# Performance work log

Hardware: AMD Instinct MI355X
Metric: run time of the kernel (lower is better)

The kernel has to match this reference:

```python
import jax, jax.numpy as jnp
import numpy as np

THRESHOLD = 0.7


def ternary_dequant(w, threshold=THRESHOLD):
    """Ternary quantize {-1,0,+1} with masked-mean alpha, return ternary*alpha."""
    abs_w = jnp.abs(w)
    delta = threshold * jnp.mean(abs_w)
    ternary = jnp.where(w > delta, 1.0, jnp.where(w < -delta, -1.0, 0.0)).astype(w.dtype)
    nz = ternary != 0
    cnt = jnp.sum(nz)
    # alpha = mean(|w| over nonzero ternary entries); fall back to mean(|w|) if all-zero
    masked_sum = jnp.sum(jnp.where(nz, abs_w, 0.0))
    alpha = jnp.where(cnt > 0, masked_sum / jnp.maximum(cnt, 1).astype(w.dtype), jnp.mean(abs_w))
    return ternary * alpha


def setup_inputs() -> dict:
    key = jax.random.key(0)
    kx, kw, kb = jax.random.split(key, 3)
    B, S, D_IN, D_OUT = 4, 2048, 4096, 4096
    x = jax.random.normal(kx, (B * S, D_IN), dtype=jnp.float32)
    # xavier-uniform-ish init for latent FP32 weights
    limit = np.sqrt(6.0 / (D_IN + D_OUT)).astype(np.float32)
    weight = jax.random.uniform(kw, (D_OUT, D_IN), dtype=jnp.float32, minval=-limit, maxval=limit)
    bias = jax.random.normal(kb, (D_OUT,), dtype=jnp.float32) * 0.02
    return {"x": x, "weight": weight, "bias": bias}


def reference(x, weight, bias):
    q_weight = ternary_dequant(weight)  # (out, in)
    return jnp.matmul(x, q_weight.T) + bias  # (tokens, out)
```

## Files before the change

### kernel.cpp

```cpp
#include <hip/hip_runtime.h>

#define M_DIM 8192
#define N_DIM 4096
#define K_DIM 4096

typedef __attribute__((ext_vector_type(8))) __bf16 bf16x8;
typedef __attribute__((ext_vector_type(4))) __bf16 bf16x4;
typedef __attribute__((ext_vector_type(4))) float floatx4;

__device__ __forceinline__ void async_copy16(const void* g, void* l) {
    __builtin_amdgcn_global_load_lds(
        (const __attribute__((address_space(1))) void*)g,
        (__attribute__((address_space(3))) void*)l,
        16, 0, 0);
}

__device__ __forceinline__ unsigned lds_addr(const void* p) {
    return (unsigned)(unsigned long long)(const __attribute__((address_space(3))) void*)p;
}
__device__ __forceinline__ bf16x8 lds_read_b128(unsigned addr) {
    bf16x8 r;
    asm volatile("ds_read_b128 %0, %1" : "=v"(r) : "v"(addr));
    return r;
}

__device__ __forceinline__ double wave_reduce_d(double v) {
    #pragma unroll
    for (int o = 32; o > 0; o >>= 1) v += __shfl_down(v, o, 64);
    return v;
}
__device__ __forceinline__ unsigned wave_reduce_u(unsigned v) {
    #pragma unroll
    for (int o = 32; o > 0; o >>= 1) v += __shfl_down(v, o, 64);
    return v;
}

__global__ __launch_bounds__(256) void k_pre(const float4* __restrict__ w4,
                                             double* __restrict__ part,
                                             const float4* __restrict__ x4,
                                             bf16x4* __restrict__ xb) {
    const int tid = threadIdx.x;
    if (blockIdx.x < 2048) {
        int idx = blockIdx.x * 256 + tid;
        double s = 0.0;
        #pragma unroll
        for (int it = 0; it < 8; ++it) {
            float4 v = w4[idx + it * (2048 * 256)];
            s += (double)fabsf(v.x) + (double)fabsf(v.y) +
                 (double)fabsf(v.z) + (double)fabsf(v.w);
        }
        s = wave_reduce_d(s);
        __shared__ double sm[4];
        if ((tid & 63) == 0) sm[tid >> 6] = s;
        __syncthreads();
        if (tid == 0) part[blockIdx.x] = sm[0] + sm[1] + sm[2] + sm[3];
    } else {
        int idx = (blockIdx.x - 2048) * 256 + tid;
        #pragma unroll
        for (int it = 0; it < 4; ++it) {
            int i = idx + it * (8192 * 256);
            float4 v = x4[i];
            bf16x4 o;
            o[0] = (__bf16)v.x; o[1] = (__bf16)v.y;
            o[2] = (__bf16)v.z; o[3] = (__bf16)v.w;
            xb[i] = o;
        }
    }
}

__global__ __launch_bounds__(256) void k_quant(const float4* __restrict__ w4,
                                               bf16x4* __restrict__ tern,
                                               const double* __restrict__ part,
                                               double* __restrict__ scal,
                                               double* __restrict__ pm,
                                               unsigned* __restrict__ pc) {
    const int tid = threadIdx.x;
    double s = 0.0;
    #pragma unroll
    for (int i = 0; i < 8; ++i) s += part[tid + i * 256];
    s = wave_reduce_d(s);
    __shared__ double sm[4];
    if ((tid & 63) == 0) sm[tid >> 6] = s;
    __syncthreads();
    const double mean = (sm[0] + sm[1] + sm[2] + sm[3]) * (1.0 / 16777216.0);
    const double delta = 0.7 * mean;
    if (blockIdx.x == 0 && tid == 0) scal[0] = mean;

    int idx = blockIdx.x * 256 + tid;
    double msum = 0.0;
    unsigned cnt = 0;
    #pragma unroll
    for (int it = 0; it < 8; ++it) {
        int i = idx + it * (2048 * 256);
        float4 v = w4[i];
        float e[4] = {v.x, v.y, v.z, v.w};
        bf16x4 o;
        #pragma unroll
        for (int c = 0; c < 4; ++c) {
            float wv = e[c];
            float t = ((double)wv > delta) ? 1.0f
                    : (((double)wv < -delta) ? -1.0f : 0.0f);
            if (t != 0.0f) { msum += (double)fabsf(wv); cnt++; }
            o[c] = (__bf16)t;
        }
        tern[i] = o;
    }
    msum = wave_reduce_d(msum);
    cnt  = wave_reduce_u(cnt);
    __shared__ double smd[4];
    __shared__ unsigned smu[4];
    if ((tid & 63) == 0) { smd[tid >> 6] = msum; smu[tid >> 6] = cnt; }
    __syncthreads();
    if (tid == 0) {
        pm[blockIdx.x] = smd[0] + smd[1] + smd[2] + smd[3];
        pc[blockIdx.x] = smu[0] + smu[1] + smu[2] + smu[3];
    }
}

__global__ __launch_bounds__(512, 2) void ternary_gemm(
    const __bf16* __restrict__ A,
    const __bf16* __restrict__ B,
    const float*  __restrict__ bias,
    const double* __restrict__ scal,
    const double* __restrict__ pm,
    const unsigned* __restrict__ pc,
    float* __restrict__ C)
{
    __shared__ __attribute__((aligned(128))) __bf16 As[4][8192];
    __shared__ __attribute__((aligned(128))) __bf16 Bs[4][8192];
    __shared__ double smd[8];
    __shared__ unsigned smu[8];

    const int tid  = threadIdx.x;
    const int w    = tid >> 6;
    const int lane = tid & 63;
    const int quad = lane >> 4;
    const int l16  = lane & 15;
    const int wr = w >> 2;
    const int wc = w & 3;

    const int id = (blockIdx.x & 7) * 64 + (blockIdx.x >> 3);
    const int br = id >> 4;
    const int bc = id & 15;

    const int srow = lane >> 2;
    const int scol = ((lane & 3) ^ ((srow >> 1) & 3)) * 8;

    const __bf16* gA0 = A + (size_t)(br * 256 + w * 16 + srow) * K_DIM + scol;
    const __bf16* gA1 = gA0 + (size_t)128 * K_DIM;
    const __bf16* gB0 = B + (size_t)(bc * 256 + w * 16 + srow) * K_DIM + scol;
    const __bf16* gB1 = gB0 + (size_t)128 * K_DIM;

    floatx4 acc[8][4] = {};

    const int swz   = (quad ^ ((l16 >> 1) & 3)) * 8;
    const int a_off = (wr * 128 + l16) * 32 + swz;
    const int b_off = (wc * 64 + l16) * 32 + swz;

    const unsigned aAddr0 = lds_addr(&As[0][0]) + (unsigned)(a_off * 2);
    const unsigned bAddr0 = lds_addr(&Bs[0][0]) + (unsigned)(b_off * 2);

#define STAGE_A(ktt) do {                                        \
        const int _sb = (ktt) & 3; const int _so = (ktt) * 32;   \
        async_copy16(gA0 + _so, &As[_sb][w * 512]);              \
        async_copy16(gA1 + _so, &As[_sb][(w + 8) * 512]);        \
    } while (0)
#define STAGE_B(ktt) do {                                        \
        const int _sb = (ktt) & 3; const int _so = (ktt) * 32;   \
        async_copy16(gB0 + _so, &Bs[_sb][w * 512]);              \
        async_copy16(gB1 + _so, &Bs[_sb][(w + 8) * 512]);        \
    } while (0)

    STAGE_A(0); STAGE_B(0);
    STAGE_A(1); STAGE_B(1);
    STAGE_A(2); STAGE_B(2);

#define TILE(kt_, VMN, DO_STAGE_) do {                                         \
        asm volatile("s_waitcnt vmcnt(" #VMN ")" ::: "memory");                \
        __builtin_amdgcn_s_barrier();                                          \
        const unsigned _bufB = (unsigned)(((kt_) & 3) * 16384);                \
        bf16x8 _a[8], _b[4];                                                   \
        _Pragma("unroll")                                                      \
        for (int i = 0; i < 4; ++i)                                            \
            _a[i] = lds_read_b128(aAddr0 + _bufB + (unsigned)(i * 1024));      \
        _Pragma("unroll")                                                      \
        for (int j = 0; j < 4; ++j)                                            \
            _b[j] = lds_read_b128(bAddr0 + _bufB + (unsigned)(j * 1024));      \
        _Pragma("unroll")                                                      \
        for (int i = 4; i < 8; ++i)                                            \
            _a[i] = lds_read_b128(aAddr0 + _bufB + (unsigned)(i * 1024));      \
        if (DO_STAGE_) { STAGE_A((kt_) + 3); STAGE_B((kt_) + 3); }             \
        asm volatile("s_waitcnt lgkmcnt(4)" ::: "memory");                     \
        __builtin_amdgcn_sched_barrier(0);                                     \
        __builtin_amdgcn_s_setprio(1);                                         \
        _Pragma("unroll")                                                      \
        for (int i = 0; i < 4; ++i)                                            \
            _Pragma("unroll")                                                  \
            for (int j = 0; j < 4; ++j)                                        \
                acc[i][j] = __builtin_amdgcn_mfma_f32_16x16x32_bf16(           \
                    _a[i], _b[j], acc[i][j], 0, 0, 0);                         \
        __builtin_amdgcn_s_setprio(0);                                         \
        asm volatile("s_waitcnt lgkmcnt(0)" ::: "memory");                     \
        __builtin_amdgcn_sched_barrier(0);                                     \
        __builtin_amdgcn_s_setprio(1);                                         \
        _Pragma("unroll")                                                      \
        for (int i = 0; i < 4; ++i)                                            \
            _Pragma("unroll")                                                  \
            for (int j = 0; j < 4; ++j)                                        \
                acc[4 + i][j] = __builtin_amdgcn_mfma_f32_16x16x32_bf16(       \
                    _a[4 + i], _b[j], acc[4 + i][j], 0, 0, 0);                 \
        __builtin_amdgcn_s_setprio(0);                                         \
        __builtin_amdgcn_sched_barrier(0);                                     \
    } while (0)

    for (int kt = 0; kt < 125; ++kt) TILE(kt, 8, true);
    TILE(125, 8, false);
    TILE(126, 4, false);
    TILE(127, 0, false);

#undef TILE
#undef STAGE_A
#undef STAGE_B

    double s = 0.0; unsigned c = 0;
    #pragma unroll
    for (int i = 0; i < 4; ++i) { s += pm[tid + i * 512]; c += pc[tid + i * 512]; }
    s = wave_reduce_d(s);
    c = wave_reduce_u(c);
    if (lane == 0) { smd[w] = s; smu[w] = c; }
    __syncthreads();
    double ms = 0.0; unsigned ct = 0;
    #pragma unroll
    for (int i = 0; i < 8; ++i) { ms += smd[i]; ct += smu[i]; }
    const float alpha = (float)(ct > 0 ? ms / (double)ct : scal[0]);

    float bv[4];
    #pragma unroll
    for (int j = 0; j < 4; ++j)
        bv[j] = bias[bc * 256 + wc * 64 + j * 16 + l16];

    #pragma unroll
    for (int i = 0; i < 8; ++i) {
        const int row0 = br * 256 + wr * 128 + i * 16 + quad * 4;
        #pragma unroll
        for (int j = 0; j < 4; ++j) {
            const int col = bc * 256 + wc * 64 + j * 16 + l16;
            #pragma unroll
            for (int r = 0; r < 4; ++r)
                C[(size_t)(row0 + r) * N_DIM + col] = acc[i][j][r] * alpha + bv[j];
        }
    }
}

extern "C" void kernel_launch(void* const* d_in, const int* in_sizes, int n_in,
                              void* d_out, int out_size, void* d_ws, size_t ws_size,
                              hipStream_t stream) {
    const float* x    = (const float*)d_in[0];
    const float* w    = (const float*)d_in[1];
    const float* bias = (const float*)d_in[2];
    float* out = (float*)d_out;

    char* ws = (char*)d_ws;
    double*   d_scal = (double*)ws;
    double*   part   = (double*)(ws + 64);
    double*   pm     = (double*)(ws + 16448);
    unsigned* pc     = (unsigned*)(ws + 32832);
    __bf16*   xb     = (__bf16*)(ws + 65536);
    __bf16*   tern   = (__bf16*)(ws + 65536 + (size_t)M_DIM * K_DIM * 2);

    k_pre<<<10240, 256, 0, stream>>>((const float4*)w, part, (const float4*)x, (bf16x4*)xb);
    k_quant<<<2048, 256, 0, stream>>>((const float4*)w, (bf16x4*)tern, part, d_scal, pm, pc);

    dim3 grid(512);
    ternary_gemm<<<grid, 512, 0, stream>>>(xb, tern, bias, d_scal, pm, pc, out);
}
```

Before: 516.3 us.

## Shrink GEMM tile to 256x128 with 4 waves and 3-stage LDS pipeline

Changes the GEMM block tile from 256x256 with 8 waves to 256x128 with 4 waves over 1024 blocks. The LDS ring drops from 4 to 3 stages, with staging issued at the top of each tile and a second barrier at the end of each tile. LDS reads now use immediate offsets instead of computed addresses. Smaller LDS use per block may let more blocks fit per CU, but each block reuses A less, so more bytes of A are fetched per unit of compute, and the extra barrier adds sync cost.

```diff
diff --git a/kernel.cpp b/kernel.cpp
--- a/kernel.cpp
+++ b/kernel.cpp
@@ -18,11 +18,8 @@
 __device__ __forceinline__ unsigned lds_addr(const void* p) {
     return (unsigned)(unsigned long long)(const __attribute__((address_space(3))) void*)p;
 }
-__device__ __forceinline__ bf16x8 lds_read_b128(unsigned addr) {
-    bf16x8 r;
-    asm volatile("ds_read_b128 %0, %1" : "=v"(r) : "v"(addr));
-    return r;
-}
+#define DSR(dst, addr, OFF) \
+    asm volatile("ds_read_b128 %0, %1 offset:" #OFF : "=v"(dst) : "v"(addr))
 
 __device__ __forceinline__ double wave_reduce_d(double v) {
     #pragma unroll
@@ -117,7 +114,7 @@
     }
 }
 
-__global__ __launch_bounds__(512, 2) void ternary_gemm(
+__global__ __launch_bounds__(256, 2) void ternary_gemm(
     const __bf16* __restrict__ A,
     const __bf16* __restrict__ B,
     const float*  __restrict__ bias,
@@ -126,30 +123,34 @@
     const unsigned* __restrict__ pc,
     float* __restrict__ C)
 {
-    __shared__ __attribute__((aligned(128))) __bf16 As[4][8192];
-    __shared__ __attribute__((aligned(128))) __bf16 Bs[4][8192];
-    __shared__ double smd[8];
-    __shared__ unsigned smu[8];
+    __shared__ __attribute__((aligned(128))) __bf16 As[3][8192];
+    __shared__ __attribute__((aligned(128))) __bf16 Bs[3][4096];
+    __shared__ double smd[4];
+    __shared__ unsigned smu[4];
 
     const int tid  = threadIdx.x;
     const int w    = tid >> 6;
     const int lane = tid & 63;
     const int quad = lane >> 4;
     const int l16  = lane & 15;
-    const int wr = w >> 2;
-    const int wc = w & 3;
-
-    const int id = (blockIdx.x & 7) * 64 + (blockIdx.x >> 3);
-    const int br = id >> 4;
-    const int bc = id & 15;
+    const int wr = w >> 1;
+    const int wc = w & 1;
+
+    const int id = (blockIdx.x & 7) * 128 + (blockIdx.x >> 3);
+    const int br = id >> 5;
+    const int bc = id & 31;
 
     const int srow = lane >> 2;
     const int scol = ((lane & 3) ^ ((srow >> 1) & 3)) * 8;
 
-    const __bf16* gA0 = A + (size_t)(br * 256 + w * 16 + srow) * K_DIM + scol;
-    const __bf16* gA1 = gA0 + (size_t)128 * K_DIM;
-    const __bf16* gB0 = B + (size_t)(bc * 256 + w * 16 + srow) * K_DIM + scol;
-    const __bf16* gB1 = gB0 + (size_t)128 * K_DIM;
+    const __bf16* gA[4];
+    const __bf16* gB[2];
+    #pragma unroll
+    for (int t = 0; t < 4; ++t)
+        gA[t] = A + (size_t)(br * 256 + (w * 4 + t) * 16 + srow) * K_DIM + scol;
+    #pragma unroll
+    for (int t = 0; t < 2; ++t)
+        gB[t] = B + (size_t)(bc * 128 + (w * 2 + t) * 16 + srow) * K_DIM + scol;
 
     floatx4 acc[8][4] = {};
 
@@ -157,39 +158,34 @@
     const int a_off = (wr * 128 + l16) * 32 + swz;
     const int b_off = (wc * 64 + l16) * 32 + swz;
 
-    const unsigned aAddr0 = lds_addr(&As[0][0]) + (unsigned)(a_off * 2);
-    const unsigned bAddr0 = lds_addr(&Bs[0][0]) + (unsigned)(b_off * 2);
-
-#define STAGE_A(ktt) do {                                        \
-        const int _sb = (ktt) & 3; const int _so = (ktt) * 32;   \
-        async_copy16(gA0 + _so, &As[_sb][w * 512]);              \
-        async_copy16(gA1 + _so, &As[_sb][(w + 8) * 512]);        \
+    const unsigned aS0 = lds_addr(&As[0][0]) + (unsigned)(a_off * 2);
+    const unsigned aS1 = aS0 + 16384;
+    const unsigned aS2 = aS0 + 32768;
+    const unsigned bS0 = lds_addr(&Bs[0][0]) + (unsigned)(b_off * 2);
+    const unsigned bS1 = bS0 + 8192;
+    const unsigned bS2 = bS0 + 16384;
+
+#define STAGE(stg, SLOT) do {                                              \
+        const int _so = (stg) * 32;                                        \
+        async_copy16(gA[0] + _so, &As[SLOT][(w * 4 + 0) * 512]);           \
+        async_copy16(gA[1] + _so, &As[SLOT][(w * 4 + 1) * 512]);           \
+        async_copy16(gA[2] + _so, &As[SLOT][(w * 4 + 2) * 512]);           \
+        async_copy16(gA[3] + _so, &As[SLOT][(w * 4 + 3) * 512]);           \
+        async_copy16(gB[0] + _so, &Bs[SLOT][(w * 2 + 0) * 512]);           \
+        async_copy16(gB[1] + _so, &Bs[SLOT][(w * 2 + 1) * 512]);           \
     } while (0)
-#define STAGE_B(ktt) do {                                        \
-        const int _sb = (ktt) & 3; const int _so = (ktt) * 32;   \
-        async_copy16(gB0 + _so, &Bs[_sb][w * 512]);              \
-        async_copy16(gB1 + _so, &Bs[_sb][(w + 8) * 512]);        \
-    } while (0)
-
-    STAGE_A(0); STAGE_B(0);
-    STAGE_A(1); STAGE_B(1);
-    STAGE_A(2); STAGE_B(2);
-
-#define TILE(kt_, VMN, DO_STAGE_) do {                                         \
+
+#define TILE(stg, SSLOT, AB, BB, VMN, DO_STAGE) do {                           \
+        if (DO_STAGE) STAGE(stg, SSLOT);                                       \
         asm volatile("s_waitcnt vmcnt(" #VMN ")" ::: "memory");                \
         __builtin_amdgcn_s_barrier();                                          \
-        const unsigned _bufB = (unsigned)(((kt_) & 3) * 16384);                \
         bf16x8 _a[8], _b[4];                                                   \
-        _Pragma("unroll")                                                      \
-        for (int i = 0; i < 4; ++i)                                            \
-            _a[i] = lds_read_b128(aAddr0 + _bufB + (unsigned)(i * 1024));      \
-        _Pragma("unroll")                                                      \
-        for (int j = 0; j < 4; ++j)                                            \
-            _b[j] = lds_read_b128(bAddr0 + _bufB + (unsigned)(j * 1024));      \
-        _Pragma("unroll")                                                      \
-        for (int i = 4; i < 8; ++i)                                            \
-            _a[i] = lds_read_b128(aAddr0 + _bufB + (unsigned)(i * 1024));      \
-        if (DO_STAGE_) { STAGE_A((kt_) + 3); STAGE_B((kt_) + 3); }             \
+        DSR(_a[0], AB, 0);    DSR(_a[1], AB, 1024);                            \
+        DSR(_a[2], AB, 2048); DSR(_a[3], AB, 3072);                            \
+        DSR(_b[0], BB, 0);    DSR(_b[1], BB, 1024);                            \
+        DSR(_b[2], BB, 2048); DSR(_b[3], BB, 3072);                            \
+        DSR(_a[4], AB, 4096); DSR(_a[5], AB, 5120);                            \
+        DSR(_a[6], AB, 6144); DSR(_a[7], AB, 7168);                            \
         asm volatile("s_waitcnt lgkmcnt(4)" ::: "memory");                     \
         __builtin_amdgcn_sched_barrier(0);                                     \
         __builtin_amdgcn_s_setprio(1);                                         \
@@ -211,40 +207,45 @@
                     _a[4 + i], _b[j], acc[4 + i][j], 0, 0, 0);                 \
         __builtin_amdgcn_s_setprio(0);                                         \
         __builtin_amdgcn_sched_barrier(0);                                     \
+        __builtin_amdgcn_s_barrier();                                          \
     } while (0)
 
-    for (int kt = 0; kt < 125; ++kt) TILE(kt, 8, true);
-    TILE(125, 8, false);
-    TILE(126, 4, false);
-    TILE(127, 0, false);
+    STAGE(0, 0);
+    STAGE(1, 1);
+
+    for (int kt = 0; kt < 126; kt += 3) {
+        TILE(kt + 2, 2, aS0, bS0, 12, true);
+        TILE(kt + 3, 0, aS1, bS1, 12, true);
+        TILE(kt + 4, 1, aS2, bS2, 12, true);
+    }
+    TILE(0, 0, aS0, bS0, 6, false);
+    TILE(0, 0, aS1, bS1, 0, false);
 
 #undef TILE
-#undef STAGE_A
-#undef STAGE_B
+#undef STAGE
 
     double s = 0.0; unsigned c = 0;
     #pragma unroll
-    for (int i = 0; i < 4; ++i) { s += pm[tid + i * 512]; c += pc[tid + i * 512]; }
+    for (int i = 0; i < 8; ++i) { s += pm[tid + i * 256]; c += pc[tid + i * 256]; }
     s = wave_reduce_d(s);
     c = wave_reduce_u(c);
-    if (lane == 0) { smd[w] = s; smu[w] = c; }
+    if ((tid & 63) == 0) { smd[tid >> 6] = s; smu[tid >> 6] = c; }
     __syncthreads();
-    double ms = 0.0; unsigned ct = 0;
-    #pragma unroll
-    for (int i = 0; i < 8; ++i) { ms += smd[i]; ct += smu[i]; }
+    const double ms = smd[0] + smd[1] + smd[2] + smd[3];
+    const unsigned ct = smu[0] + smu[1] + smu[2] + smu[3];
     const float alpha = (float)(ct > 0 ? ms / (double)ct : scal[0]);
 
     float bv[4];
     #pragma unroll
     for (int j = 0; j < 4; ++j)
-        bv[j] = bias[bc * 256 + wc * 64 + j * 16 + l16];
+        bv[j] = bias[bc * 128 + wc * 64 + j * 16 + l16];
 
     #pragma unroll
     for (int i = 0; i < 8; ++i) {
         const int row0 = br * 256 + wr * 128 + i * 16 + quad * 4;
         #pragma unroll
         for (int j = 0; j < 4; ++j) {
-            const int col = bc * 256 + wc * 64 + j * 16 + l16;
+            const int col = bc * 128 + wc * 64 + j * 16 + l16;
             #pragma unroll
             for (int r = 0; r < 4; ++r)
                 C[(size_t)(row0 + r) * N_DIM + col] = acc[i][j][r] * alpha + bv[j];
@@ -271,6 +272,5 @@
     k_pre<<<10240, 256, 0, stream>>>((const float4*)w, part, (const float4*)x, (bf16x4*)xb);
     k_quant<<<2048, 256, 0, stream>>>((const float4*)w, (bf16x4*)tern, part, d_scal, pm, pc);
 
-    dim3 grid(512);
-    ternary_gemm<<<grid, 512, 0, stream>>>(xb, tern, bias, d_scal, pm, pc, out);
-}
+    ternary_gemm<<<1024, 256, 0, stream>>>(xb, tern, bias, d_scal, pm, pc, out);
+}
```

New measurement: 562.3 us. 8.9% more time.

## Software-pipeline LDS fragment reads with register double-buffering across MFMA groups

Applied to the files above, without the earlier changes.

The GEMM main loop now double-buffers A/B fragments in registers (rA0/rA1, rB0/rB1). The next tile's ds_read_b128 loads and the global-to-LDS staging are interleaved between groups of MFMAs of the current tile, using immediate LDS offsets. The aim is to hide LDS read latency behind matrix math instead of waiting on it at the start of each tile. The wave-to-row staging assignment is also remapped so each wave stages two adjacent 16-row blocks. This raises register pressure and depends on tight waitcnt and barrier ordering being correct.

```diff
diff --git a/kernel.cpp b/kernel.cpp
--- a/kernel.cpp
+++ b/kernel.cpp
@@ -18,11 +18,12 @@
 __device__ __forceinline__ unsigned lds_addr(const void* p) {
     return (unsigned)(unsigned long long)(const __attribute__((address_space(3))) void*)p;
 }
-__device__ __forceinline__ bf16x8 lds_read_b128(unsigned addr) {
-    bf16x8 r;
-    asm volatile("ds_read_b128 %0, %1" : "=v"(r) : "v"(addr));
-    return r;
-}
+#define DSRD(dst, addr, OFF) \
+    asm volatile("ds_read_b128 %0, %1 offset:" #OFF : "=v"(dst) : "v"(addr))
+
+#define SB  __builtin_amdgcn_sched_barrier(0)
+#define SP1 __builtin_amdgcn_s_setprio(1)
+#define SP0 __builtin_amdgcn_s_setprio(0)
 
 __device__ __forceinline__ double wave_reduce_d(double v) {
     #pragma unroll
@@ -146,81 +147,108 @@
     const int srow = lane >> 2;
     const int scol = ((lane & 3) ^ ((srow >> 1) & 3)) * 8;
 
-    const __bf16* gA0 = A + (size_t)(br * 256 + w * 16 + srow) * K_DIM + scol;
-    const __bf16* gA1 = gA0 + (size_t)128 * K_DIM;
-    const __bf16* gB0 = B + (size_t)(bc * 256 + w * 16 + srow) * K_DIM + scol;
-    const __bf16* gB1 = gB0 + (size_t)128 * K_DIM;
+    const __bf16* gA0 = A + (size_t)(br * 256 + (2 * w + 0) * 16 + srow) * K_DIM + scol;
+    const __bf16* gA1 = A + (size_t)(br * 256 + (2 * w + 1) * 16 + srow) * K_DIM + scol;
+    const __bf16* gB0 = B + (size_t)(bc * 256 + (2 * w + 0) * 16 + srow) * K_DIM + scol;
+    const __bf16* gB1 = B + (size_t)(bc * 256 + (2 * w + 1) * 16 + srow) * K_DIM + scol;
 
     floatx4 acc[8][4] = {};
 
     const int swz   = (quad ^ ((l16 >> 1) & 3)) * 8;
-    const int a_off = (wr * 128 + l16) * 32 + swz;
-    const int b_off = (wc * 64 + l16) * 32 + swz;
-
-    const unsigned aAddr0 = lds_addr(&As[0][0]) + (unsigned)(a_off * 2);
-    const unsigned bAddr0 = lds_addr(&Bs[0][0]) + (unsigned)(b_off * 2);
-
-#define STAGE_A(ktt) do {                                        \
-        const int _sb = (ktt) & 3; const int _so = (ktt) * 32;   \
-        async_copy16(gA0 + _so, &As[_sb][w * 512]);              \
-        async_copy16(gA1 + _so, &As[_sb][(w + 8) * 512]);        \
+    const int a_off = (wr * 128 + l16) * 64 + swz * 2;
+    const int b_off = (wc * 64  + l16) * 64 + swz * 2;
+
+    const unsigned aS0 = lds_addr(&As[0][0]) + (unsigned)a_off;
+    const unsigned aS1 = aS0 + 16384;
+    const unsigned aS2 = aS0 + 32768;
+    const unsigned aS3 = aS0 + 49152;
+    const unsigned bS0 = lds_addr(&Bs[0][0]) + (unsigned)b_off;
+    const unsigned bS1 = bS0 + 16384;
+    const unsigned bS2 = bS0 + 32768;
+    const unsigned bS3 = bS0 + 49152;
+
+    bf16x8 rA0[8], rA1[8], rB0[4], rB1[4];
+
+#define STAGE2A(stg_, SLOT) do {                                   \
+        const int _so = (stg_) * 32;                               \
+        async_copy16(gA0 + _so, &As[SLOT][(2 * w + 0) * 512]);     \
+        async_copy16(gA1 + _so, &As[SLOT][(2 * w + 1) * 512]);     \
     } while (0)
-#define STAGE_B(ktt) do {                                        \
-        const int _sb = (ktt) & 3; const int _so = (ktt) * 32;   \
-        async_copy16(gB0 + _so, &Bs[_sb][w * 512]);              \
-        async_copy16(gB1 + _so, &Bs[_sb][(w + 8) * 512]);        \
+#define STAGE2B(stg_, SLOT) do {                                   \
+        const int _so = (stg_) * 32;                               \
+        async_copy16(gB0 + _so, &Bs[SLOT][(2 * w + 0) * 512]);     \
+        async_copy16(gB1 + _so, &Bs[SLOT][(2 * w + 1) * 512]);     \
     } while (0)
 
-    STAGE_A(0); STAGE_B(0);
-    STAGE_A(1); STAGE_B(1);
-    STAGE_A(2); STAGE_B(2);
-
-#define TILE(kt_, VMN, DO_STAGE_) do {                                         \
+#define MF4(CUR, I) do {                                                        \
+        acc[I][0] = __builtin_amdgcn_mfma_f32_16x16x32_bf16(rA##CUR[I], rB##CUR[0], acc[I][0], 0, 0, 0); \
+        acc[I][1] = __builtin_amdgcn_mfma_f32_16x16x32_bf16(rA##CUR[I], rB##CUR[1], acc[I][1], 0, 0, 0); \
+        acc[I][2] = __builtin_amdgcn_mfma_f32_16x16x32_bf16(rA##CUR[I], rB##CUR[2], acc[I][2], 0, 0, 0); \
+        acc[I][3] = __builtin_amdgcn_mfma_f32_16x16x32_bf16(rA##CUR[I], rB##CUR[3], acc[I][3], 0, 0, 0); \
+    } while (0)
+
+#define ITER(AN, BN, SSLOT, CUR, NXT, stg_, VMN, DO_DSR, DO_STAGE) do {        \
         asm volatile("s_waitcnt vmcnt(" #VMN ")" ::: "memory");                \
         __builtin_amdgcn_s_barrier();                                          \
-        const unsigned _bufB = (unsigned)(((kt_) & 3) * 16384);                \
-        bf16x8 _a[8], _b[4];                                                   \
-        _Pragma("unroll")                                                      \
-        for (int i = 0; i < 4; ++i)                                            \
-            _a[i] = lds_read_b128(aAddr0 + _bufB + (unsigned)(i * 1024));      \
-        _Pragma("unroll")                                                      \
-        for (int j = 0; j < 4; ++j)                                            \
-            _b[j] = lds_read_b128(bAddr0 + _bufB + (unsigned)(j * 1024));      \
-        _Pragma("unroll")                                                      \
-        for (int i = 4; i < 8; ++i)                                            \
-            _a[i] = lds_read_b128(aAddr0 + _bufB + (unsigned)(i * 1024));      \
-        if (DO_STAGE_) { STAGE_A((kt_) + 3); STAGE_B((kt_) + 3); }             \
-        asm volatile("s_waitcnt lgkmcnt(4)" ::: "memory");                     \
-        __builtin_amdgcn_sched_barrier(0);                                     \
-        __builtin_amdgcn_s_setprio(1);                                         \
-        _Pragma("unroll")                                                      \
-        for (int i = 0; i < 4; ++i)                                            \
-            _Pragma("unroll")                                                  \
-            for (int j = 0; j < 4; ++j)                                        \
-                acc[i][j] = __builtin_amdgcn_mfma_f32_16x16x32_bf16(           \
-                    _a[i], _b[j], acc[i][j], 0, 0, 0);                         \
-        __builtin_amdgcn_s_setprio(0);                                         \
         asm volatile("s_waitcnt lgkmcnt(0)" ::: "memory");                     \
-        __builtin_amdgcn_sched_barrier(0);                                     \
-        __builtin_amdgcn_s_setprio(1);                                         \
-        _Pragma("unroll")                                                      \
-        for (int i = 0; i < 4; ++i)                                            \
-            _Pragma("unroll")                                                  \
-            for (int j = 0; j < 4; ++j)                                        \
-                acc[4 + i][j] = __builtin_amdgcn_mfma_f32_16x16x32_bf16(       \
-                    _a[4 + i], _b[j], acc[4 + i][j], 0, 0, 0);                 \
-        __builtin_amdgcn_s_setprio(0);                                         \
-        __builtin_amdgcn_sched_barrier(0);                                     \
+        SB;                                                                    \
+        SP1; MF4(CUR, 0); SP0; SB;                                             \
+        if (DO_DSR) { DSRD(rA##NXT[0], AN, 0);                                 \
+                      DSRD(rA##NXT[1], AN, 1024);                              \
+                      DSRD(rA##NXT[2], AN, 2048); }                            \
+        SB;                                                                    \
+        SP1; MF4(CUR, 1); SP0; SB;                                             \
+        if (DO_DSR) { DSRD(rA##NXT[3], AN, 3072);                              \
+                      DSRD(rB##NXT[0], BN, 0);                                 \
+                      DSRD(rB##NXT[1], BN, 1024); }                            \
+        SB;                                                                    \
+        SP1; MF4(CUR, 2); SP0; SB;                                             \
+        if (DO_DSR) { DSRD(rB##NXT[2], BN, 2048);                              \
+                      DSRD(rB##NXT[3], BN, 3072);                              \
+                      DSRD(rA##NXT[4], AN, 4096); }                            \
+        SB;                                                                    \
+        SP1; MF4(CUR, 3); SP0; SB;                                             \
+        if (DO_DSR) { DSRD(rA##NXT[5], AN, 5120);                              \
+                      DSRD(rA##NXT[6], AN, 6144);                              \
+                      DSRD(rA##NXT[7], AN, 7168); }                            \
+        SB;                                                                    \
+        SP1; MF4(CUR, 4); SP0; SB;                                             \
+        if (DO_STAGE) STAGE2A(stg_, SSLOT);                                    \
+        SB;                                                                    \
+        SP1; MF4(CUR, 5); SP0; SB;                                             \
+        if (DO_STAGE) STAGE2B(stg_, SSLOT);                                    \
+        SB;                                                                    \
+        SP1; MF4(CUR, 6); MF4(CUR, 7); SP0;                                    \
+        SB;                                                                    \
     } while (0)
 
-    for (int kt = 0; kt < 125; ++kt) TILE(kt, 8, true);
-    TILE(125, 8, false);
-    TILE(126, 4, false);
-    TILE(127, 0, false);
-
-#undef TILE
-#undef STAGE_A
-#undef STAGE_B
+    STAGE2A(0, 0); STAGE2B(0, 0);
+    STAGE2A(1, 1); STAGE2B(1, 1);
+    STAGE2A(2, 2); STAGE2B(2, 2);
+    asm volatile("s_waitcnt vmcnt(8)" ::: "memory");
+    __builtin_amdgcn_s_barrier();
+    DSRD(rA0[0], aS0, 0);    DSRD(rA0[1], aS0, 1024);
+    DSRD(rA0[2], aS0, 2048); DSRD(rA0[3], aS0, 3072);
+    DSRD(rA0[4], aS0, 4096); DSRD(rA0[5], aS0, 5120);
+    DSRD(rA0[6], aS0, 6144); DSRD(rA0[7], aS0, 7168);
+    DSRD(rB0[0], bS0, 0);    DSRD(rB0[1], bS0, 1024);
+    DSRD(rB0[2], bS0, 2048); DSRD(rB0[3], bS0, 3072);
+
+    for (int n = 0; n < 124; n += 4) {
+        ITER(aS1, bS1, 3, 0, 1, n + 3, 4, 1, 1);
+        ITER(aS2, bS2, 0, 1, 0, n + 4, 4, 1, 1);
+        ITER(aS3, bS3, 1, 0, 1, n + 5, 4, 1, 1);
+        ITER(aS0, bS0, 2, 1, 0, n + 6, 4, 1, 1);
+    }
+    ITER(aS1, bS1, 3, 0, 1, 127, 4, 1, 1);
+    ITER(aS2, bS2, 0, 1, 0, 0,   4, 1, 0);
+    ITER(aS3, bS3, 0, 0, 1, 0,   0, 1, 0);
+    ITER(aS0, bS0, 0, 1, 0, 0,   0, 0, 0);
+
+#undef ITER
+#undef MF4
+#undef STAGE2A
+#undef STAGE2B
 
     double s = 0.0; unsigned c = 0;
     #pragma unroll
@@ -271,6 +299,5 @@
     k_pre<<<10240, 256, 0, stream>>>((const float4*)w, part, (const float4*)x, (bf16x4*)xb);
     k_quant<<<2048, 256, 0, stream>>>((const float4*)w, (bf16x4*)tern, part, d_scal, pm, pc);
 
-    dim3 grid(512);
-    ternary_gemm<<<grid, 512, 0, stream>>>(xb, tern, bias, d_scal, pm, pc, out);
-}
+    ternary_gemm<<<512, 512, 0, stream>>>(xb, tern, bias, d_scal, pm, pc, out);
+}
```

New measurement: 618.8 us. +19.9%, slower.
